# Kernel tuning notes

Measured on AMD Instinct MI355X. Metric: run time of the kernel, lower is better.

Reference implementation:

```python
import jax, jax.numpy as jnp
import numpy as np

K = 0.5  # bottom-k fraction from __init__


def setup_inputs() -> dict:
    key = jax.random.key(0)
    k1, k2 = jax.random.split(key)
    N, V = 8192, 32000
    outputs = jax.random.normal(k1, (N, V), dtype=jnp.float32)
    labels = jax.random.randint(k2, (N,), 0, V, dtype=jnp.int64)
    return {"outputs": outputs, "labels": labels}


def reference(outputs, labels):
    # per-sample cross entropy: logsumexp(logits) - logits[label]
    N = outputs.shape[0]
    logZ = jax.nn.logsumexp(outputs, axis=-1)                             # [N]
    picked = jnp.take_along_axis(outputs, labels[:, None], axis=-1)[:, 0]  # [N]
    ce = logZ - picked                                                     # [N]
    m = int(N * K)  # number of smallest losses kept (K in (0,1])
    # bottom-k via top_k on negated losses (avoids full sort)
    neg_bottom, _ = jax.lax.top_k(-ce, m)
    return jnp.mean(-neg_bottom)
```

## Files before the change

### kernel.cpp

```cpp
#include <hip/hip_runtime.h>
#include <math.h>


#define MAX_N 8192

typedef float f32x4 __attribute__((ext_vector_type(4)));

__global__ __launch_bounds__(256) void ce_rows(const float* __restrict__ logits,
                                               const int* __restrict__ labels,
                                               float* __restrict__ ce, int n, int V) {
    const int lane = threadIdx.x & 63;
    const int wid = threadIdx.x >> 6;
    const int row = blockIdx.x * 4 + wid;
    if (row >= n) return;

    const float* rp = logits + (size_t)row * V;
    const f32x4* rp4 = (const f32x4*)rp;
    const int V4 = V >> 2;

    float s0 = 0.f, s1 = 0.f, s2 = 0.f, s3 = 0.f;
    float s4 = 0.f, s5 = 0.f, s6 = 0.f, s7 = 0.f;
    int j = lane;
    for (; j + 64 < V4; j += 128) {
        f32x4 a = __builtin_nontemporal_load(&rp4[j]);
        f32x4 b = __builtin_nontemporal_load(&rp4[j + 64]);
        s0 += __expf(a.x); s1 += __expf(a.y); s2 += __expf(a.z); s3 += __expf(a.w);
        s4 += __expf(b.x); s5 += __expf(b.y); s6 += __expf(b.z); s7 += __expf(b.w);
    }
    for (; j < V4; j += 64) {
        f32x4 a = __builtin_nontemporal_load(&rp4[j]);
        s0 += __expf(a.x); s1 += __expf(a.y); s2 += __expf(a.z); s3 += __expf(a.w);
    }
    for (int t = (V4 << 2) + lane; t < V; t += 64) s0 += __expf(rp[t]);

    float s = ((s0 + s1) + (s2 + s3)) + ((s4 + s5) + (s6 + s7));
    #pragma unroll
    for (int off = 32; off > 0; off >>= 1) s += __shfl_down(s, off, 64);

    if (lane == 0) {
        float picked = rp[labels[row]];
        ce[row] = __logf(s) - picked;
    }
}

__device__ __forceinline__ unsigned f2k(float f) {
    unsigned u = __float_as_uint(f);
    return (u & 0x80000000u) ? ~u : (u | 0x80000000u);
}
__device__ __forceinline__ float k2f(unsigned k) {
    unsigned u = (k & 0x80000000u) ? (k ^ 0x80000000u) : ~k;
    return __uint_as_float(u);
}

__global__ __launch_bounds__(1024) void bottomk_mean(const float* __restrict__ ce,
                                                     float* __restrict__ out,
                                                     int n, int m) {
    __shared__ unsigned keys[MAX_N];
    __shared__ unsigned hist[256];
    __shared__ unsigned s_prefix, s_remaining;
    const int tid = threadIdx.x;

    for (int i = tid; i < n; i += 1024) keys[i] = f2k(ce[i]);
    if (tid == 0) { s_prefix = 0u; s_remaining = (unsigned)m; }
    __syncthreads();

    unsigned prefmask = 0u;
    for (int shift = 24; shift >= 0; shift -= 8) {
        if (tid < 256) hist[tid] = 0u;
        __syncthreads();
        const unsigned prefix = s_prefix;
        for (int i = tid; i < n; i += 1024) {
            unsigned k = keys[i];
            if ((k & prefmask) == prefix) atomicAdd(&hist[(k >> shift) & 255u], 1u);
        }
        __syncthreads();
        if (tid == 0) {
            unsigned rem = s_remaining, cum = 0u;
            int b = 0;
            for (; b < 256; ++b) {
                if (cum + hist[b] >= rem) break;
                cum += hist[b];
            }
            s_prefix = prefix | ((unsigned)b << shift);
            s_remaining = rem - cum;
        }
        prefmask |= (255u << shift);
        __syncthreads();
    }

    const unsigned T = s_prefix;
    float lsum = 0.f;
    unsigned lcnt = 0u;
    for (int i = tid; i < n; i += 1024) {
        unsigned k = keys[i];
        if (k < T) { lsum += k2f(k); lcnt++; }
    }
    #pragma unroll
    for (int off = 32; off > 0; off >>= 1) {
        lsum += __shfl_down(lsum, off, 64);
        lcnt += __shfl_down(lcnt, off, 64);
    }
    __shared__ float wsum[16];
    __shared__ unsigned wcnt[16];
    const int lane = tid & 63, wid = tid >> 6;
    if (lane == 0) { wsum[wid] = lsum; wcnt[wid] = lcnt; }
    __syncthreads();
    if (tid == 0) {
        float tot = 0.f;
        unsigned cnt = 0u;
        const int nw = (1024 + 63) / 64;
        for (int w = 0; w < nw; ++w) { tot += wsum[w]; cnt += wcnt[w]; }
        tot += (float)((unsigned)m - cnt) * k2f(T);
        out[0] = tot / (float)m;
    }
}

extern "C" void kernel_launch(void* const* d_in, const int* in_sizes, int n_in,
                              void* d_out, int out_size, void* d_ws, size_t ws_size,
                              hipStream_t stream) {
    const float* logits = (const float*)d_in[0];
    const int* labels = (const int*)d_in[1];
    float* out = (float*)d_out;
    float* ce = (float*)d_ws;

    const int N = in_sizes[1];
    const int V = in_sizes[0] / N;
    const int M = N / 2;

    const int rows_per_block = 4;
    ce_rows<<<(N + rows_per_block - 1) / rows_per_block, 256, 0, stream>>>(logits, labels, ce, N, V);
    bottomk_mean<<<1, 1024, 0, stream>>>(ce, out, N, M);
}
```

Baseline: 210.9 us.

## Fuse per-row cross-entropy and bottom-k selection via last-block-done pattern

```diff
diff --git a/kernel.cpp b/kernel.cpp
--- a/kernel.cpp
+++ b/kernel.cpp
@@ -3,74 +3,98 @@
 
 
 #define MAX_N 8192
+#define KPT 32
 
 typedef float f32x4 __attribute__((ext_vector_type(4)));
 
-__global__ __launch_bounds__(256) void ce_rows(const float* __restrict__ logits,
-                                               const int* __restrict__ labels,
-                                               float* __restrict__ ce, int n, int V) {
-    const int lane = threadIdx.x & 63;
-    const int wid = threadIdx.x >> 6;
-    const int row = blockIdx.x * 4 + wid;
-    if (row >= n) return;
-
-    const float* rp = logits + (size_t)row * V;
-    const f32x4* rp4 = (const f32x4*)rp;
-    const int V4 = V >> 2;
-
-    float s0 = 0.f, s1 = 0.f, s2 = 0.f, s3 = 0.f;
-    float s4 = 0.f, s5 = 0.f, s6 = 0.f, s7 = 0.f;
-    int j = lane;
-    for (; j + 64 < V4; j += 128) {
-        f32x4 a = __builtin_nontemporal_load(&rp4[j]);
-        f32x4 b = __builtin_nontemporal_load(&rp4[j + 64]);
-        s0 += __expf(a.x); s1 += __expf(a.y); s2 += __expf(a.z); s3 += __expf(a.w);
-        s4 += __expf(b.x); s5 += __expf(b.y); s6 += __expf(b.z); s7 += __expf(b.w);
-    }
-    for (; j < V4; j += 64) {
-        f32x4 a = __builtin_nontemporal_load(&rp4[j]);
-        s0 += __expf(a.x); s1 += __expf(a.y); s2 += __expf(a.z); s3 += __expf(a.w);
-    }
-    for (int t = (V4 << 2) + lane; t < V; t += 64) s0 += __expf(rp[t]);
-
-    float s = ((s0 + s1) + (s2 + s3)) + ((s4 + s5) + (s6 + s7));
-    #pragma unroll
-    for (int off = 32; off > 0; off >>= 1) s += __shfl_down(s, off, 64);
-
-    if (lane == 0) {
-        float picked = rp[labels[row]];
-        ce[row] = __logf(s) - picked;
-    }
-}
-
-__device__ __forceinline__ unsigned f2k(float f) {
-    unsigned u = __float_as_uint(f);
-    return (u & 0x80000000u) ? ~u : (u | 0x80000000u);
-}
 __device__ __forceinline__ float k2f(unsigned k) {
     unsigned u = (k & 0x80000000u) ? (k ^ 0x80000000u) : ~k;
     return __uint_as_float(u);
 }
 
-__global__ __launch_bounds__(1024) void bottomk_mean(const float* __restrict__ ce,
-                                                     float* __restrict__ out,
-                                                     int n, int m) {
-    __shared__ unsigned keys[MAX_N];
+__global__ __launch_bounds__(256) void fused_ce_bottomk(
+    const float* __restrict__ logits, const int* __restrict__ labels,
+    float* __restrict__ ce, unsigned* __restrict__ counter,
+    float* __restrict__ out, int n, int V, int m)
+{
+    const int lane = threadIdx.x & 63;
+    const int wid  = threadIdx.x >> 6;
+    const int row  = blockIdx.x * 4 + wid;
+
+    if (row < n) {
+        const float* rp = logits + (size_t)row * V;
+        const f32x4* rp4 = (const f32x4*)rp;
+        const int V4 = V >> 2;
+
+        float s0=0,s1=0,s2=0,s3=0,s4=0,s5=0,s6=0,s7=0;
+        float s8=0,s9=0,sa=0,sb=0,sc=0,sd=0,se=0,sf=0;
+        int j = lane;
+        for (; j + 192 < V4; j += 256) {
+            f32x4 a = __builtin_nontemporal_load(&rp4[j]);
+            f32x4 b = __builtin_nontemporal_load(&rp4[j + 64]);
+            f32x4 c = __builtin_nontemporal_load(&rp4[j + 128]);
+            f32x4 d = __builtin_nontemporal_load(&rp4[j + 192]);
+            s0 += __expf(a.x); s1 += __expf(a.y); s2 += __expf(a.z); s3 += __expf(a.w);
+            s4 += __expf(b.x); s5 += __expf(b.y); s6 += __expf(b.z); s7 += __expf(b.w);
+            s8 += __expf(c.x); s9 += __expf(c.y); sa += __expf(c.z); sb += __expf(c.w);
+            sc += __expf(d.x); sd += __expf(d.y); se += __expf(d.z); sf += __expf(d.w);
+        }
+        for (; j < V4; j += 64) {
+            f32x4 a = __builtin_nontemporal_load(&rp4[j]);
+            s0 += __expf(a.x); s1 += __expf(a.y); s2 += __expf(a.z); s3 += __expf(a.w);
+        }
+        for (int t = (V4 << 2) + lane; t < V; t += 64) s0 += __expf(rp[t]);
+
+        float s = (((s0+s1)+(s2+s3)) + ((s4+s5)+(s6+s7)))
+                + (((s8+s9)+(sa+sb)) + ((sc+sd)+(se+sf)));
+        #pragma unroll
+        for (int off = 32; off > 0; off >>= 1) s += __shfl_down(s, off, 64);
+
+        if (lane == 0) {
+            float picked = rp[labels[row]];
+            ce[row] = __logf(s) - picked;
+            __threadfence();
+        }
+    }
+
+    __shared__ unsigned s_last;
+    __syncthreads();
+    if (threadIdx.x == 0) {
+        unsigned old = __hip_atomic_fetch_add(counter, 1u, __ATOMIC_ACQ_REL,
+                                              __HIP_MEMORY_SCOPE_AGENT);
+        s_last = (old == gridDim.x - 1) ? 1u : 0u;
+    }
+    __syncthreads();
+    if (!s_last) return;
+
+    const int tid = threadIdx.x;
+    const unsigned* ceu = (const unsigned*)ce;
+
+    unsigned kreg[KPT];
+    #pragma unroll
+    for (int p = 0; p < KPT; ++p) {
+        int i = tid + p * 256;
+        if (i < n) {
+            unsigned u = __hip_atomic_load(&ceu[i], __ATOMIC_RELAXED,
+                                           __HIP_MEMORY_SCOPE_AGENT);
+            kreg[p] = (u & 0x80000000u) ? ~u : (u | 0x80000000u);
+        } else {
+            kreg[p] = 0xFFFFFFFFu;
+        }
+    }
+
     __shared__ unsigned hist[256];
     __shared__ unsigned s_prefix, s_remaining;
-    const int tid = threadIdx.x;
-
-    for (int i = tid; i < n; i += 1024) keys[i] = f2k(ce[i]);
     if (tid == 0) { s_prefix = 0u; s_remaining = (unsigned)m; }
-    __syncthreads();
 
     unsigned prefmask = 0u;
     for (int shift = 24; shift >= 0; shift -= 8) {
-        if (tid < 256) hist[tid] = 0u;
+        hist[tid] = 0u;
         __syncthreads();
         const unsigned prefix = s_prefix;
-        for (int i = tid; i < n; i += 1024) {
-            unsigned k = keys[i];
+        #pragma unroll
+        for (int p = 0; p < KPT; ++p) {
+            unsigned k = kreg[p];
             if ((k & prefmask) == prefix) atomicAdd(&hist[(k >> shift) & 255u], 1u);
         }
         __syncthreads();
@@ -78,8 +102,9 @@
             unsigned rem = s_remaining, cum = 0u;
             int b = 0;
             for (; b < 256; ++b) {
-                if (cum + hist[b] >= rem) break;
-                cum += hist[b];
+                unsigned h = hist[b];
+                if (cum + h >= rem) break;
+                cum += h;
             }
             s_prefix = prefix | ((unsigned)b << shift);
             s_remaining = rem - cum;
@@ -91,8 +116,9 @@
     const unsigned T = s_prefix;
     float lsum = 0.f;
     unsigned lcnt = 0u;
-    for (int i = tid; i < n; i += 1024) {
-        unsigned k = keys[i];
+    #pragma unroll
+    for (int p = 0; p < KPT; ++p) {
+        unsigned k = kreg[p];
         if (k < T) { lsum += k2f(k); lcnt++; }
     }
     #pragma unroll
@@ -100,16 +126,13 @@
         lsum += __shfl_down(lsum, off, 64);
         lcnt += __shfl_down(lcnt, off, 64);
     }
-    __shared__ float wsum[16];
-    __shared__ unsigned wcnt[16];
-    const int lane = tid & 63, wid = tid >> 6;
+    __shared__ float wsum[4];
+    __shared__ unsigned wcnt[4];
     if (lane == 0) { wsum[wid] = lsum; wcnt[wid] = lcnt; }
     __syncthreads();
     if (tid == 0) {
-        float tot = 0.f;
-        unsigned cnt = 0u;
-        const int nw = (1024 + 63) / 64;
-        for (int w = 0; w < nw; ++w) { tot += wsum[w]; cnt += wcnt[w]; }
+        float tot = (wsum[0] + wsum[1]) + (wsum[2] + wsum[3]);
+        unsigned cnt = (wcnt[0] + wcnt[1]) + (wcnt[2] + wcnt[3]);
         tot += (float)((unsigned)m - cnt) * k2f(T);
         out[0] = tot / (float)m;
     }
@@ -122,12 +145,14 @@
     const int* labels = (const int*)d_in[1];
     float* out = (float*)d_out;
     float* ce = (float*)d_ws;
+    unsigned* counter = (unsigned*)((char*)d_ws + 32768);
 
     const int N = in_sizes[1];
     const int V = in_sizes[0] / N;
     const int M = N / 2;
 
-    const int rows_per_block = 4;
-    ce_rows<<<(N + rows_per_block - 1) / rows_per_block, 256, 0, stream>>>(logits, labels, ce, N, V);
-    bottomk_mean<<<1, 1024, 0, stream>>>(ce, out, N, M);
+    hipMemsetAsync(counter, 0, sizeof(unsigned), stream);
+    const int blocks = (N + 3) / 4;
+    fused_ce_bottomk<<<blocks, 256, 0, stream>>>(logits, labels, ce, counter,
+                                                 out, N, V, M);
 }
```

New measurement: 664.7 us. 215% more time.

## Keep radix-select keys in registers and parallelize bucket scan; drop nontemporal loads

Applied to the files above, without the earlier changes.

```diff
diff --git a/kernel.cpp b/kernel.cpp
--- a/kernel.cpp
+++ b/kernel.cpp
@@ -3,8 +3,18 @@
 
 
 #define MAX_N 8192
+#define KPT 32
 
 typedef float f32x4 __attribute__((ext_vector_type(4)));
+
+__device__ __forceinline__ unsigned f2k(float f) {
+    unsigned u = __float_as_uint(f);
+    return (u & 0x80000000u) ? ~u : (u | 0x80000000u);
+}
+__device__ __forceinline__ float k2f(unsigned k) {
+    unsigned u = (k & 0x80000000u) ? (k ^ 0x80000000u) : ~k;
+    return __uint_as_float(u);
+}
 
 __global__ __launch_bounds__(256) void ce_rows(const float* __restrict__ logits,
                                                const int* __restrict__ labels,
@@ -22,13 +32,13 @@
     float s4 = 0.f, s5 = 0.f, s6 = 0.f, s7 = 0.f;
     int j = lane;
     for (; j + 64 < V4; j += 128) {
-        f32x4 a = __builtin_nontemporal_load(&rp4[j]);
-        f32x4 b = __builtin_nontemporal_load(&rp4[j + 64]);
+        f32x4 a = rp4[j];
+        f32x4 b = rp4[j + 64];
         s0 += __expf(a.x); s1 += __expf(a.y); s2 += __expf(a.z); s3 += __expf(a.w);
         s4 += __expf(b.x); s5 += __expf(b.y); s6 += __expf(b.z); s7 += __expf(b.w);
     }
     for (; j < V4; j += 64) {
-        f32x4 a = __builtin_nontemporal_load(&rp4[j]);
+        f32x4 a = rp4[j];
         s0 += __expf(a.x); s1 += __expf(a.y); s2 += __expf(a.z); s3 += __expf(a.w);
     }
     for (int t = (V4 << 2) + lane; t < V; t += 64) s0 += __expf(rp[t]);
@@ -43,46 +53,51 @@
     }
 }
 
-__device__ __forceinline__ unsigned f2k(float f) {
-    unsigned u = __float_as_uint(f);
-    return (u & 0x80000000u) ? ~u : (u | 0x80000000u);
-}
-__device__ __forceinline__ float k2f(unsigned k) {
-    unsigned u = (k & 0x80000000u) ? (k ^ 0x80000000u) : ~k;
-    return __uint_as_float(u);
-}
+__global__ __launch_bounds__(256) void bottomk_mean(const float* __restrict__ ce,
+                                                    float* __restrict__ out,
+                                                    int n, int m) {
+    const int tid = threadIdx.x;
+    const int lane = tid & 63, wid = tid >> 6;
 
-__global__ __launch_bounds__(1024) void bottomk_mean(const float* __restrict__ ce,
-                                                     float* __restrict__ out,
-                                                     int n, int m) {
-    __shared__ unsigned keys[MAX_N];
+    unsigned kreg[KPT];
+    #pragma unroll
+    for (int p = 0; p < KPT; ++p) {
+        int i = tid + p * 256;
+        kreg[p] = (i < n) ? f2k(ce[i]) : 0xFFFFFFFFu;
+    }
+
     __shared__ unsigned hist[256];
+    __shared__ unsigned scan[256];
     __shared__ unsigned s_prefix, s_remaining;
-    const int tid = threadIdx.x;
-
-    for (int i = tid; i < n; i += 1024) keys[i] = f2k(ce[i]);
     if (tid == 0) { s_prefix = 0u; s_remaining = (unsigned)m; }
-    __syncthreads();
 
     unsigned prefmask = 0u;
     for (int shift = 24; shift >= 0; shift -= 8) {
-        if (tid < 256) hist[tid] = 0u;
+        hist[tid] = 0u;
         __syncthreads();
         const unsigned prefix = s_prefix;
-        for (int i = tid; i < n; i += 1024) {
-            unsigned k = keys[i];
+        const unsigned rem = s_remaining;
+        #pragma unroll
+        for (int p = 0; p < KPT; ++p) {
+            unsigned k = kreg[p];
             if ((k & prefmask) == prefix) atomicAdd(&hist[(k >> shift) & 255u], 1u);
         }
         __syncthreads();
-        if (tid == 0) {
-            unsigned rem = s_remaining, cum = 0u;
-            int b = 0;
-            for (; b < 256; ++b) {
-                if (cum + hist[b] >= rem) break;
-                cum += hist[b];
-            }
-            s_prefix = prefix | ((unsigned)b << shift);
-            s_remaining = rem - cum;
+        unsigned h = hist[tid];
+        scan[tid] = h;
+        __syncthreads();
+        #pragma unroll
+        for (int off = 1; off < 256; off <<= 1) {
+            unsigned t = (tid >= off) ? scan[tid - off] : 0u;
+            __syncthreads();
+            scan[tid] += t;
+            __syncthreads();
+        }
+        unsigned incl = scan[tid];
+        unsigned excl = incl - h;
+        if (excl < rem && incl >= rem) {
+            s_prefix = prefix | ((unsigned)tid << shift);
+            s_remaining = rem - excl;
         }
         prefmask |= (255u << shift);
         __syncthreads();
@@ -91,8 +106,9 @@
     const unsigned T = s_prefix;
     float lsum = 0.f;
     unsigned lcnt = 0u;
-    for (int i = tid; i < n; i += 1024) {
-        unsigned k = keys[i];
+    #pragma unroll
+    for (int p = 0; p < KPT; ++p) {
+        unsigned k = kreg[p];
         if (k < T) { lsum += k2f(k); lcnt++; }
     }
     #pragma unroll
@@ -100,16 +116,13 @@
         lsum += __shfl_down(lsum, off, 64);
         lcnt += __shfl_down(lcnt, off, 64);
     }
-    __shared__ float wsum[16];
-    __shared__ unsigned wcnt[16];
-    const int lane = tid & 63, wid = tid >> 6;
+    __shared__ float wsum[4];
+    __shared__ unsigned wcnt[4];
     if (lane == 0) { wsum[wid] = lsum; wcnt[wid] = lcnt; }
     __syncthreads();
     if (tid == 0) {
-        float tot = 0.f;
-        unsigned cnt = 0u;
-        const int nw = (1024 + 63) / 64;
-        for (int w = 0; w < nw; ++w) { tot += wsum[w]; cnt += wcnt[w]; }
+        float tot = (wsum[0] + wsum[1]) + (wsum[2] + wsum[3]);
+        unsigned cnt = (wcnt[0] + wcnt[1]) + (wcnt[2] + wcnt[3]);
         tot += (float)((unsigned)m - cnt) * k2f(T);
         out[0] = tot / (float)m;
     }
@@ -129,5 +142,5 @@
 
     const int rows_per_block = 4;
     ce_rows<<<(N + rows_per_block - 1) / rows_per_block, 256, 0, stream>>>(logits, labels, ce, N, V);
-    bottomk_mean<<<1, 1024, 0, stream>>>(ce, out, N, M);
+    bottomk_mean<<<1, 256, 0, stream>>>(ce, out, N, M);
 }
```

New measurement: 211.7 us. No clear change (+0.4%).
